# Kernel optimization log

Measured on AMD Instinct MI355X. Metric: run time of the kernel, lower is better.

Reference implementation:

```python
import jax, jax.numpy as jnp
import numpy as np

S = 30.0
M = 0.4
EPS = 1e-07


def setup_inputs() -> dict:
    key = jax.random.key(0)
    k1, k2, k3 = jax.random.split(key, 3)
    B, D, C = 1024, 512, 50000
    x = jax.random.normal(k1, (B, D), dtype=jnp.float32)
    labels = jax.random.randint(k2, (B,), 0, C, dtype=jnp.int64)
    W = jax.random.normal(k3, (C, D), dtype=jnp.float32) * 0.02
    return {"x": x, "labels": labels, "W": W}


def reference(x, labels, W):
    # NOTE: original torch code's weight-normalization loop is a no-op
    # (rebinds a local), so W is used unnormalized. Only x is normalized.
    xn = x / jnp.maximum(jnp.linalg.norm(x, axis=1, keepdims=True), 1e-12)
    cos_theta = xn @ W.T  # [B, C]

    B = x.shape[0]
    rows = jnp.arange(B)
    target = cos_theta[rows, labels]  # [B]
    target = jnp.clip(target, -1.0 + EPS, 1.0 - EPS)
    numerator = S * jnp.cos(jnp.arccos(target) + M)  # [B]

    # sum of exp(s * cos) over all classes except the true one
    exp_all = jnp.exp(S * cos_theta)  # [B, C]
    excl_sum = jnp.sum(exp_all, axis=1) - exp_all[rows, labels]  # [B]

    denominator = jnp.exp(numerator) + excl_sum
    loss = numerator - jnp.log(denominator)
    return (cos_theta, -jnp.mean(loss))
```

## Files before the change

kernel.cpp:

```cpp
#include <hip/hip_runtime.h>
#include <hip/hip_bf16.h>
#include <math.h>


#define DD 512
#define TM 128
#define TN 128
#define TK 32
#define NSTEP (DD / TK)

typedef __attribute__((ext_vector_type(8))) short short8;
typedef __attribute__((ext_vector_type(4))) float f32x4;

__global__ __launch_bounds__(256) void arc_normalize_bf16(const float* __restrict__ x,
                                                          __hip_bfloat16* __restrict__ xn,
                                                          float* __restrict__ sumexp,
                                                          int B) {
    int r = blockIdx.x;
    int tid = threadIdx.x;
    const float* xr = x + (size_t)r * DD;
    float v0 = xr[tid];
    float v1 = xr[tid + 256];
    float ss = v0 * v0 + v1 * v1;
    #pragma unroll
    for (int off = 32; off > 0; off >>= 1) ss += __shfl_down(ss, off, 64);
    __shared__ float wsum[4];
    if ((tid & 63) == 0) wsum[tid >> 6] = ss;
    __syncthreads();
    float tot = wsum[0] + wsum[1] + wsum[2] + wsum[3];
    float inv = 1.0f / fmaxf(sqrtf(tot), 1e-12f);
    xn[(size_t)r * DD + tid] = __float2bfloat16(v0 * inv);
    xn[(size_t)r * DD + tid + 256] = __float2bfloat16(v1 * inv);
    if (tid == 0) sumexp[r] = 0.0f;
}

__global__ __launch_bounds__(256) void arc_cvt_w(const float* __restrict__ W,
                                                 __hip_bfloat16* __restrict__ Wb,
                                                 long n) {
    long i = ((long)blockIdx.x * 256 + threadIdx.x) * 8;
    if (i + 8 <= n) {
        f32x4 a = __builtin_nontemporal_load((const f32x4*)(W + i));
        f32x4 b = __builtin_nontemporal_load((const f32x4*)(W + i + 4));
        union { __hip_bfloat16 h[8]; short8 v; } pk;
        pk.h[0] = __float2bfloat16(a.x); pk.h[1] = __float2bfloat16(a.y);
        pk.h[2] = __float2bfloat16(a.z); pk.h[3] = __float2bfloat16(a.w);
        pk.h[4] = __float2bfloat16(b.x); pk.h[5] = __float2bfloat16(b.y);
        pk.h[6] = __float2bfloat16(b.z); pk.h[7] = __float2bfloat16(b.w);
        *(short8*)(Wb + i) = pk.v;
    } else if (i < n) {
        for (long j = i; j < n; j++) Wb[j] = __float2bfloat16(W[j]);
    }
}

__global__ __launch_bounds__(256) void arc_gemm_mfma(const __hip_bfloat16* __restrict__ A,
                                                     const __hip_bfloat16* __restrict__ Wb,
                                                     float* __restrict__ out,
                                                     float* __restrict__ sumexp,
                                                     int C) {
    __shared__ __hip_bfloat16 Als[2][TM * TK];
    __shared__ __hip_bfloat16 Bls[2][TN * TK];

    const int tid = threadIdx.x;
    const int lane = tid & 63;
    const int wave = tid >> 6;
    const int quad = lane >> 4;
    const int l16 = lane & 15;
    const int wm = (wave >> 1) * 64;
    const int wn = (wave & 1) * 64;

    const int nwg = gridDim.x * gridDim.y;
    const int flat = blockIdx.x + gridDim.x * blockIdx.y;
    const int xcd = flat & 7;
    const int pos = flat >> 3;
    const int q = nwg >> 3;
    const int r8 = nwg & 7;
    const int wg = (xcd < r8 ? xcd * (q + 1) : r8 * (q + 1) + (xcd - r8) * q) + pos;
    const int m0 = (wg % gridDim.x) * TM;
    const int n0 = (wg / gridDim.x) * TN;

    f32x4 acc[4][4];
    #pragma unroll
    for (int i = 0; i < 4; i++)
        #pragma unroll
        for (int j = 0; j < 4; j++) acc[i][j] = (f32x4){0.f, 0.f, 0.f, 0.f};

    const int rowA = tid >> 2, ch = tid & 3;
    const __hip_bfloat16* gA0 = A + (size_t)(m0 + rowA) * DD + ch * 8;
    const __hip_bfloat16* gA1 = gA0 + (size_t)64 * DD;
    int nr0 = n0 + rowA;      if (nr0 >= C) nr0 = C - 1;
    int nr1 = n0 + 64 + rowA; if (nr1 >= C) nr1 = C - 1;
    const __hip_bfloat16* gB0 = Wb + (size_t)nr0 * DD + ch * 8;
    const __hip_bfloat16* gB1 = Wb + (size_t)nr1 * DD + ch * 8;

    const int ldsOff = (tid & ~63) * 16;

#define ISSUE(t, buf)                                                                \
    do {                                                                             \
        char* dA_ = (char*)&Als[(buf)][0] + ldsOff;                                  \
        char* dB_ = (char*)&Bls[(buf)][0] + ldsOff;                                  \
        __builtin_amdgcn_global_load_lds(                                            \
            (const __attribute__((address_space(1))) void*)(gA0 + (t) * TK),         \
            (__attribute__((address_space(3))) void*)dA_, 16, 0, 0);                 \
        __builtin_amdgcn_global_load_lds(                                            \
            (const __attribute__((address_space(1))) void*)(gA1 + (t) * TK),         \
            (__attribute__((address_space(3))) void*)(dA_ + 4096), 16, 0, 0);        \
        __builtin_amdgcn_global_load_lds(                                            \
            (const __attribute__((address_space(1))) void*)(gB0 + (t) * TK),         \
            (__attribute__((address_space(3))) void*)dB_, 16, 0, 0);                 \
        __builtin_amdgcn_global_load_lds(                                            \
            (const __attribute__((address_space(1))) void*)(gB1 + (t) * TK),         \
            (__attribute__((address_space(3))) void*)(dB_ + 4096), 16, 0, 0);        \
    } while (0)

    ISSUE(0, 0);

    for (int t = 0; t < NSTEP; t++) {
        const int cur = t & 1, nxt = cur ^ 1;
        __syncthreads();

        if (t + 1 < NSTEP) ISSUE(t + 1, nxt);

        short8 af[4], bfr[4];
        #pragma unroll
        for (int mi = 0; mi < 4; mi++)
            af[mi] = *(const short8*)((const char*)&Als[cur][0] +
                                      ((wm + mi * 16 + l16) * TK + quad * 8) * 2);
        #pragma unroll
        for (int ni = 0; ni < 4; ni++)
            bfr[ni] = *(const short8*)((const char*)&Bls[cur][0] +
                                       ((wn + ni * 16 + l16) * TK + quad * 8) * 2);

        #pragma unroll
        for (int mi = 0; mi < 4; mi++)
            #pragma unroll
            for (int ni = 0; ni < 4; ni++)
                acc[mi][ni] = __builtin_amdgcn_mfma_f32_16x16x32_bf16(
                    af[mi], bfr[ni], acc[mi][ni], 0, 0, 0);
    }
#undef ISSUE

    const bool full = (n0 + TN <= C);
    #pragma unroll
    for (int mi = 0; mi < 4; mi++) {
        float se[4] = {0.f, 0.f, 0.f, 0.f};
        #pragma unroll
        for (int ni = 0; ni < 4; ni++) {
            int n = n0 + wn + ni * 16 + l16;
            f32x4 v = acc[mi][ni];
            if (full || n < C) {
                size_t base = (size_t)(m0 + wm + mi * 16 + quad * 4) * C + n;
                #pragma unroll
                for (int r = 0; r < 4; r++) {
                    out[base + (size_t)r * C] = v[r];
                    se[r] += expf(30.0f * v[r]);
                }
            }
        }
        #pragma unroll
        for (int off = 1; off < 16; off <<= 1) {
            #pragma unroll
            for (int r = 0; r < 4; r++) se[r] += __shfl_xor(se[r], off, 64);
        }
        if (l16 == 0) {
            int mbase = m0 + wm + mi * 16 + quad * 4;
            #pragma unroll
            for (int r = 0; r < 4; r++) atomicAdd(&sumexp[mbase + r], se[r]);
        }
    }
}

#define BM 128
#define BN 128
#define BK 16
__global__ __launch_bounds__(256) void arc_normalize_f32(const float* __restrict__ x,
                                                         float* __restrict__ xn,
                                                         float* __restrict__ sumexp,
                                                         int B) {
    int r = blockIdx.x;
    int tid = threadIdx.x;
    const float* xr = x + (size_t)r * DD;
    float v0 = xr[tid];
    float v1 = xr[tid + 256];
    float ss = v0 * v0 + v1 * v1;
    #pragma unroll
    for (int off = 32; off > 0; off >>= 1) ss += __shfl_down(ss, off, 64);
    __shared__ float wsum[4];
    if ((tid & 63) == 0) wsum[tid >> 6] = ss;
    __syncthreads();
    float tot = wsum[0] + wsum[1] + wsum[2] + wsum[3];
    float inv = 1.0f / fmaxf(sqrtf(tot), 1e-12f);
    xn[(size_t)r * DD + tid] = v0 * inv;
    xn[(size_t)r * DD + tid + 256] = v1 * inv;
    if (tid == 0) sumexp[r] = 0.0f;
}

__global__ __launch_bounds__(256) void arc_gemm_f32(const float* __restrict__ A,
                                                    const float* __restrict__ Wm,
                                                    float* __restrict__ out,
                                                    float* __restrict__ sumexp,
                                                    int B, int C) {
    __shared__ float As[BK][BM];
    __shared__ float Bs[BK][BN];
    const int m0 = blockIdx.x * BM;
    const int n0 = blockIdx.y * BN;
    const int tid = threadIdx.x;
    const int tx = tid & 15;
    const int ty = tid >> 4;
    float acc[8][8];
    #pragma unroll
    for (int i = 0; i < 8; i++)
        #pragma unroll
        for (int j = 0; j < 8; j++) acc[i][j] = 0.0f;
    for (int k0 = 0; k0 < DD; k0 += BK) {
        #pragma unroll
        for (int l = 0; l < 2; l++) {
            int f = tid + l * 256;
            int row = f >> 2, kc = f & 3;
            float4 v = *(const float4*)(A + (size_t)(m0 + row) * DD + k0 + kc * 4);
            As[kc * 4 + 0][row] = v.x; As[kc * 4 + 1][row] = v.y;
            As[kc * 4 + 2][row] = v.z; As[kc * 4 + 3][row] = v.w;
        }
        #pragma unroll
        for (int l = 0; l < 2; l++) {
            int f = tid + l * 256;
            int row = f >> 2, kc = f & 3;
            int n = n0 + row;
            float4 v = make_float4(0.f, 0.f, 0.f, 0.f);
            if (n < C) v = *(const float4*)(Wm + (size_t)n * DD + k0 + kc * 4);
            Bs[kc * 4 + 0][row] = v.x; Bs[kc * 4 + 1][row] = v.y;
            Bs[kc * 4 + 2][row] = v.z; Bs[kc * 4 + 3][row] = v.w;
        }
        __syncthreads();
        #pragma unroll
        for (int k = 0; k < BK; k++) {
            float4 a0 = *(const float4*)&As[k][ty * 8];
            float4 a1 = *(const float4*)&As[k][ty * 8 + 4];
            float4 b0 = *(const float4*)&Bs[k][tx * 8];
            float4 b1 = *(const float4*)&Bs[k][tx * 8 + 4];
            float a[8] = {a0.x, a0.y, a0.z, a0.w, a1.x, a1.y, a1.z, a1.w};
            float b[8] = {b0.x, b0.y, b0.z, b0.w, b1.x, b1.y, b1.z, b1.w};
            #pragma unroll
            for (int i = 0; i < 8; i++)
                #pragma unroll
                for (int j = 0; j < 8; j++) acc[i][j] = fmaf(a[i], b[j], acc[i][j]);
        }
        __syncthreads();
    }
    const bool full = (n0 + BN <= C);
    #pragma unroll
    for (int i = 0; i < 8; i++) {
        int m = m0 + ty * 8 + i;
        float* orow = out + (size_t)m * C + n0 + tx * 8;
        float s = 0.0f;
        if (full) {
            *(float4*)orow = make_float4(acc[i][0], acc[i][1], acc[i][2], acc[i][3]);
            *(float4*)(orow + 4) = make_float4(acc[i][4], acc[i][5], acc[i][6], acc[i][7]);
            #pragma unroll
            for (int j = 0; j < 8; j++) s += expf(30.0f * acc[i][j]);
        } else {
            #pragma unroll
            for (int j = 0; j < 8; j++) {
                int n = n0 + tx * 8 + j;
                if (n < C) { orow[j] = acc[i][j]; s += expf(30.0f * acc[i][j]); }
            }
        }
        #pragma unroll
        for (int off = 1; off < 16; off <<= 1) s += __shfl_xor(s, off, 64);
        if (tx == 0) atomicAdd(&sumexp[m], s);
    }
}

__global__ __launch_bounds__(1024) void arc_finalize(const float* __restrict__ cosm,
                                                     const int* __restrict__ labels,
                                                     const float* __restrict__ sumexp,
                                                     float* __restrict__ out_loss,
                                                     int B, int C) {
    int r = threadIdx.x;
    float loss = 0.0f;
    if (r < B) {
        int lab = labels[r];
        float t_raw = cosm[(size_t)r * C + lab];
        float se = sumexp[r];
        float t = fminf(fmaxf(t_raw, -1.0f + 1e-7f), 1.0f - 1e-7f);
        const float cosM = 0.9210609940028851f;
        const float sinM = 0.3894183423086505f;
        float num = 30.0f * (t * cosM - sqrtf(fmaxf(1.0f - t * t, 0.0f)) * sinM);
        float excl = se - expf(30.0f * t_raw);
        float denom = expf(num) + excl;
        loss = num - logf(denom);
    }
    __shared__ float red[1024];
    red[threadIdx.x] = loss;
    __syncthreads();
    for (int s = 512; s > 0; s >>= 1) {
        if (threadIdx.x < s) red[threadIdx.x] += red[threadIdx.x + s];
        __syncthreads();
    }
    if (threadIdx.x == 0) out_loss[0] = -red[0] / (float)B;
}

extern "C" void kernel_launch(void* const* d_in, const int* in_sizes, int n_in,
                              void* d_out, int out_size, void* d_ws, size_t ws_size,
                              hipStream_t stream) {
    const float* x = (const float*)d_in[0];
    const int* labels = (const int*)d_in[1];
    const float* Wm = (const float*)d_in[2];
    int B = in_sizes[1];
    int C = in_sizes[2] / DD;
    float* out = (float*)d_out;

    size_t need = 4096 + (size_t)B * DD * 2 + (size_t)C * DD * 2 + 256;
    if (ws_size >= need) {
        float* sumexp = (float*)d_ws;
        __hip_bfloat16* xnb = (__hip_bfloat16*)((char*)d_ws + 4096);
        __hip_bfloat16* Wb = xnb + (size_t)B * DD;

        arc_normalize_bf16<<<B, 256, 0, stream>>>(x, xnb, sumexp, B);
        long wn = (long)C * DD;
        long nblk = (wn / 8 + 255) / 256;
        arc_cvt_w<<<(int)nblk, 256, 0, stream>>>(Wm, Wb, wn);
        dim3 grid(B / TM, (C + TN - 1) / TN);
        arc_gemm_mfma<<<grid, 256, 0, stream>>>(xnb, Wb, out, sumexp, C);
        arc_finalize<<<1, 1024, 0, stream>>>(out, labels, sumexp, out + (size_t)B * C, B, C);
    } else {
        float* xn = (float*)d_ws;
        float* sumexp = xn + (size_t)B * DD;
        arc_normalize_f32<<<B, 256, 0, stream>>>(x, xn, sumexp, B);
        dim3 grid(B / BM, (C + BN - 1) / BN);
        arc_gemm_f32<<<grid, 256, 0, stream>>>(xn, Wm, out, sumexp, B, C);
        arc_finalize<<<1, 1024, 0, stream>>>(out, labels, sumexp, out + (size_t)B * C, B, C);
    }
}
```

Before: 387.4 us.

## Triple-buffer LDS tiles with prefetch depth two and explicit vmcnt waits

Replaces the double-buffered A/B LDS tiles with a three-slot ring and issues global-to-LDS loads two K-steps ahead. Uses explicit s_waitcnt vmcnt with a raw s_barrier instead of __syncthreads, so the loads for step t+1 can stay in flight while step t computes. The goal is to hide global memory latency in the GEMM main loop. It costs 48KB of LDS per block, which may lower occupancy, and relies on hand-counted outstanding loads being correct.

```diff
diff --git a/kernel.cpp b/kernel.cpp
--- a/kernel.cpp
+++ b/kernel.cpp
@@ -57,8 +57,7 @@
                                                      float* __restrict__ out,
                                                      float* __restrict__ sumexp,
                                                      int C) {
-    __shared__ __hip_bfloat16 Als[2][TM * TK];
-    __shared__ __hip_bfloat16 Bls[2][TN * TK];
+    __shared__ char lds[3][16384];
 
     const int tid = threadIdx.x;
     const int lane = tid & 63;
@@ -94,10 +93,10 @@
 
     const int ldsOff = (tid & ~63) * 16;
 
-#define ISSUE(t, buf)                                                                \
+#define ISSUE(t, bufbase)                                                            \
     do {                                                                             \
-        char* dA_ = (char*)&Als[(buf)][0] + ldsOff;                                  \
-        char* dB_ = (char*)&Bls[(buf)][0] + ldsOff;                                  \
+        char* dA_ = (bufbase) + ldsOff;                                              \
+        char* dB_ = (bufbase) + 8192 + ldsOff;                                       \
         __builtin_amdgcn_global_load_lds(                                            \
             (const __attribute__((address_space(1))) void*)(gA0 + (t) * TK),         \
             (__attribute__((address_space(3))) void*)dA_, 16, 0, 0);                 \
@@ -112,23 +111,29 @@
             (__attribute__((address_space(3))) void*)(dB_ + 4096), 16, 0, 0);        \
     } while (0)
 
-    ISSUE(0, 0);
-
+    ISSUE(0, &lds[0][0]);
+    ISSUE(1, &lds[1][0]);
+
+    int ib = 0;
     for (int t = 0; t < NSTEP; t++) {
-        const int cur = t & 1, nxt = cur ^ 1;
-        __syncthreads();
-
-        if (t + 1 < NSTEP) ISSUE(t + 1, nxt);
-
+        if (t == NSTEP - 1)
+            asm volatile("s_waitcnt vmcnt(0)" ::: "memory");
+        else
+            asm volatile("s_waitcnt vmcnt(4)" ::: "memory");
+        __builtin_amdgcn_s_barrier();
+        __builtin_amdgcn_sched_barrier(0);
+
+        int ip = ib + 2; if (ip >= 3) ip -= 3;
+        if (t + 2 < NSTEP) ISSUE(t + 2, &lds[ip][0]);
+
+        const char* base = &lds[ib][0];
         short8 af[4], bfr[4];
         #pragma unroll
         for (int mi = 0; mi < 4; mi++)
-            af[mi] = *(const short8*)((const char*)&Als[cur][0] +
-                                      ((wm + mi * 16 + l16) * TK + quad * 8) * 2);
+            af[mi] = *(const short8*)(base + (wm + mi * 16 + l16) * 64 + quad * 16);
         #pragma unroll
         for (int ni = 0; ni < 4; ni++)
-            bfr[ni] = *(const short8*)((const char*)&Bls[cur][0] +
-                                       ((wn + ni * 16 + l16) * TK + quad * 8) * 2);
+            bfr[ni] = *(const short8*)(base + 8192 + (wn + ni * 16 + l16) * 64 + quad * 16);
 
         #pragma unroll
         for (int mi = 0; mi < 4; mi++)
@@ -136,6 +141,8 @@
             for (int ni = 0; ni < 4; ni++)
                 acc[mi][ni] = __builtin_amdgcn_mfma_f32_16x16x32_bf16(
                     af[mi], bfr[ni], acc[mi][ni], 0, 0, 0);
+
+        ib++; if (ib >= 3) ib -= 3;
     }
 #undef ISSUE
 
```

Result: faster. 368.7 us (-4.8%).
